# Performance work log

Measured on AMD Instinct MI355X. Metric: run time of the kernel, lower is better.

Reference implementation:

```python
import jax, jax.numpy as jnp
import numpy as np

B, S, V, E, HE, HD, MEL_D, MEL_T = 4096, 13, 276, 128, 256, 256, 80, 250

def setup_inputs() -> dict:
    key = jax.random.key(0)
    ks = jax.random.split(key, 20)
    p = lambda k, sh: (jax.random.normal(k, sh, dtype=jnp.float32) * 0.05)
    return {
        'text': jax.random.randint(ks[0], (B, S), 0, V),
        'surprisal': jax.random.normal(ks[1], (B, S), dtype=jnp.float32),
        'emb': p(ks[2], (V, E)),
        'sw': p(ks[3], (E, 1)), 'sb': p(ks[4], (E,)),
        'ew_ih': p(ks[5], (4 * HE, E)), 'ew_hh': p(ks[6], (4 * HE, HE)),
        'eb_ih': p(ks[7], (4 * HE,)), 'eb_hh': p(ks[8], (4 * HE,)),
        'aw': p(ks[9], (1, HD + HE)), 'ab': p(ks[10], (1,)),
        'dw_ih': p(ks[11], (4 * HD, E + HE)), 'dw_hh': p(ks[12], (4 * HD, HD)),
        'db_ih': p(ks[13], (4 * HD,)), 'db_hh': p(ks[14], (4 * HD,)),
        'f1w': p(ks[15], (1024, S * HD)), 'f1b': p(ks[16], (1024,)),
        'f2w': p(ks[17], (MEL_D * MEL_T, 1024)), 'f2b': p(ks[18], (MEL_D * MEL_T,)),
        'init_in': jnp.zeros((E,), dtype=jnp.float32),
    }

def _lstm_cell(x, h, c, w_ih, w_hh, b_ih, b_hh, H):
    # PyTorch gate order: i, f, g, o
    g = x @ w_ih.T + b_ih + h @ w_hh.T + b_hh
    i, f, gg, o = jnp.split(g, 4, axis=-1)
    c2 = jax.nn.sigmoid(f) * c + jax.nn.sigmoid(i) * jnp.tanh(gg)
    h2 = jax.nn.sigmoid(o) * jnp.tanh(c2)
    return h2, c2

def reference(text, surprisal, emb, sw, sb, ew_ih, ew_hh, eb_ih, eb_hh,
              aw, ab, dw_ih, dw_hh, db_ih, db_hh, f1w, f1b, f2w, f2b, init_in):
    # embedding + surprisal projection
    x = emb[text] + (surprisal[..., None] @ sw.T + sb)  # [B,S,E]

    # encoder LSTM over time
    def enc_step(carry, xt):
        h, c = carry
        h2, c2 = _lstm_cell(xt, h, c, ew_ih, ew_hh, eb_ih, eb_hh, HE)
        return (h2, c2), h2
    h0 = jnp.zeros((B, HE), dtype=x.dtype)
    (h_n, c_n), enc_seq = jax.lax.scan(enc_step, (h0, h0), jnp.swapaxes(x, 0, 1))
    enc_out = jnp.swapaxes(enc_seq, 0, 1)  # [B,S,HE]

    # precompute encoder part of attention scores (constant across steps)
    aw_h, aw_e = aw[0, :HD], aw[0, HD:]
    enc_score = enc_out @ aw_e + ab[0]  # [B,S]

    dec_in = jnp.broadcast_to(init_in, (B, E))

    def dec_step(carry, _):
        h, c = carry
        scores = h @ aw_h + 0.0  # [B]
        w = jax.nn.softmax(scores[:, None] + enc_score, axis=1)  # [B,S]
        context = jnp.einsum('bs,bsh->bh', w, enc_out)
        xcat = jnp.concatenate([dec_in, context], axis=-1)
        h2, c2 = _lstm_cell(xcat, h, c, dw_ih, dw_hh, db_ih, db_hh, HD)
        return (h2, c2), h2
    _, dec_seq = jax.lax.scan(dec_step, (h_n, c_n), None, length=S)
    dec_out = jnp.swapaxes(dec_seq, 0, 1).reshape(B, S * HD)  # [B,13*256]

    hfc = jax.nn.relu(dec_out @ f1w.T + f1b)
    out = (hfc @ f2w.T + f2b).reshape(B, MEL_D, MEL_T)
    return out
```

## Files before the change

kernel.cpp:

```cpp
#include <hip/hip_runtime.h>
#include <hip/hip_bf16.h>
#include <stdint.h>
#include <stddef.h>

#define B 4096
#define S 13
#define NG 1024
#define MEL 20000
#define MELP 20224

typedef __attribute__((ext_vector_type(8))) short bf16x8;
typedef __attribute__((ext_vector_type(4))) float f32x4;

__device__ __forceinline__ void g2l16(void* lds, const void* g) {
    __builtin_amdgcn_global_load_lds(
        (const __attribute__((address_space(1))) void*)g,
        (__attribute__((address_space(3))) void*)lds, 16, 0, 0);
}

__device__ __forceinline__ float sigm(float x) { return 1.0f / (1.0f + expf(-x)); }
__device__ __forceinline__ float b2f(unsigned short u) {
    union { float f; unsigned int i; } x; x.i = ((unsigned)u) << 16; return x.f;
}
__device__ __forceinline__ unsigned short f2bu(float f) {
    __hip_bfloat16 h = __float2bfloat16(f);
    return *reinterpret_cast<unsigned short*>(&h);
}
__device__ __forceinline__ bf16x8 cvt8(f32x4 a, f32x4 b) {
    union { bf16x8 v; __hip_bfloat16 e[8]; } u;
    #pragma unroll
    for (int j = 0; j < 4; ++j) { u.e[j] = __float2bfloat16(a[j]); u.e[4 + j] = __float2bfloat16(b[j]); }
    return u.v;
}

__device__ __forceinline__ void swz_decode(int wg, int nwg, int nx, int& bx, int& by) {
    const int cpx = nwg >> 3;
    wg = (wg & 7) * cpx + (wg >> 3);
    const int gsz = nx * 4;
    const int grp = wg / gsz, rem = wg % gsz;
    by = grp * 4 + (rem & 3);
    bx = rem >> 2;
}

#define BAR() do { asm volatile("" ::: "memory"); \
    __builtin_amdgcn_s_barrier(); \
    __builtin_amdgcn_sched_barrier(0); } while (0)

#define P_DECL() \
    __shared__ __hip_bfloat16 As3[4][128 * 32]; \
    __shared__ __hip_bfloat16 Bs3[4][64 * 32]; \
    const int tid  = threadIdx.x; \
    const int lane = tid & 63; \
    const int wv   = tid >> 6; \
    const int l16  = lane & 15; \
    const int sr   = tid >> 2; \
    const int sc   = (((tid & 3) ^ ((tid >> 3) & 3)) << 3); \
    const int sl   = (((lane >> 4) ^ ((l16 >> 1) & 3)) << 3)

#define STG3(buf, k0) do { \
    g2l16(&As3[buf][sr * 32 + (tid & 3) * 8],         Ag + (size_t)sr * K + (k0) + sc); \
    g2l16(&As3[buf][(sr + 64) * 32 + (tid & 3) * 8],  Ag + (size_t)(sr + 64) * K + (k0) + sc); \
    g2l16(&Bs3[buf][sr * 32 + (tid & 3) * 8],         Wg + (size_t)sr * K + (k0) + sc); } while (0)

#define TILE3(cur, stg, k2, DO_STG) do { \
    const __hip_bfloat16* Ab = As3[cur]; \
    const __hip_bfloat16* Bb = Bs3[cur]; \
    bf16x8 af[2], bfr[4]; \
    _Pragma("unroll") for (int m = 0; m < 2; ++m) \
        af[m] = *(const bf16x8*)(Ab + (wv * 32 + m * 16 + l16) * 32 + sl); \
    _Pragma("unroll") for (int n = 0; n < 4; ++n) \
        bfr[n] = *(const bf16x8*)(Bb + (n * 16 + l16) * 32 + sl); \
    if (DO_STG) STG3(stg, k2); \
    __builtin_amdgcn_s_setprio(1); \
    _Pragma("unroll") for (int m = 0; m < 2; ++m) \
        _Pragma("unroll") for (int n = 0; n < 4; ++n) \
            acc[m][n] = __builtin_amdgcn_mfma_f32_16x16x32_bf16(af[m], bfr[n], acc[m][n], 0, 0, 0); \
    __builtin_amdgcn_s_setprio(0); \
} while (0)

#define PIPELINE(K) do { \
    const int nk = (K) >> 5; \
    STG3(0, 0); \
    STG3(1, 32); \
    STG3(2, 64); \
    asm volatile("s_waitcnt vmcnt(6)" ::: "memory"); \
    BAR(); \
    int cur = 0; \
    for (int t = 0; t < nk - 3; ++t) { \
        const int stg = (cur + 3) & 3; \
        TILE3(cur, stg, (t + 3) << 5, true); \
        asm volatile("s_waitcnt vmcnt(6)" ::: "memory"); \
        BAR(); \
        cur = (cur + 1) & 3; \
    } \
    TILE3(cur, 0, 0, false); \
    asm volatile("s_waitcnt vmcnt(3)" ::: "memory"); \
    BAR(); \
    cur = (cur + 1) & 3; \
    TILE3(cur, 0, 0, false); \
    asm volatile("s_waitcnt vmcnt(0)" ::: "memory"); \
    BAR(); \
    cur = (cur + 1) & 3; \
    TILE3(cur, 0, 0, false); \
} while (0)

__global__ __launch_bounds__(256, 2) void gemm3(
    const __hip_bfloat16* __restrict__ A,
    const __hip_bfloat16* __restrict__ W,
    const float* __restrict__ bias,
    float* __restrict__ Cf,
    __hip_bfloat16* __restrict__ Cbf,
    int N, int K, int ldc, int relu, int nx)
{
    P_DECL();
    int bx, by;
    swz_decode(blockIdx.x, gridDim.x, nx, bx, by);
    const int brow = by * 128, bcol = bx * 64;
    const __hip_bfloat16* Ag = A + (size_t)brow * K;
    const __hip_bfloat16* Wg = W + (size_t)bcol * K;
    f32x4 acc[2][4] = {};

    PIPELINE(K);

    const int r4 = (lane >> 4) * 4;
    #pragma unroll
    for (int m = 0; m < 2; ++m) {
        #pragma unroll
        for (int n = 0; n < 4; ++n) {
            const int col = bcol + n * 16 + l16;
            if (col >= N) continue;
            const float bv = bias ? bias[col] : 0.0f;
            #pragma unroll
            for (int r = 0; r < 4; ++r) {
                const int row = brow + wv * 32 + m * 16 + r4 + r;
                float v = acc[m][n][r] + bv;
                if (relu) v = v > 0.0f ? v : 0.0f;
                if (Cf)  Cf[(size_t)row * ldc + col] = v;
                if (Cbf) Cbf[(size_t)row * ldc + col] = __float2bfloat16(v);
            }
        }
    }
}

__global__ __launch_bounds__(256, 2) void gemm_lstm3(
    const __hip_bfloat16* __restrict__ A,
    const __hip_bfloat16* __restrict__ W,
    const float* __restrict__ bias,
    float* __restrict__ c,
    float* __restrict__ hf,
    __hip_bfloat16* __restrict__ hb1, int s1,
    __hip_bfloat16* __restrict__ hb2, int s2,
    int K,
    const float* __restrict__ aw,
    float* __restrict__ score)
{
    P_DECL();
    int bx, by;
    swz_decode(blockIdx.x, gridDim.x, 16, bx, by);
    const int brow = by * 128, bcol = bx * 64;
    const __hip_bfloat16* Ag = A + (size_t)brow * K;
    const __hip_bfloat16* Wg = W + (size_t)bcol * K;
    f32x4 acc[2][4] = {};

    PIPELINE(K);

    const int r4 = (lane >> 4) * 4;
    const int unit = bx * 16 + l16;
    const float b0 = bias[bcol + l16];
    const float b1 = bias[bcol + 16 + l16];
    const float b2 = bias[bcol + 32 + l16];
    const float b3 = bias[bcol + 48 + l16];
    const float awe = score ? aw[256 + unit] : 0.0f;
    float ps[2][4];
    #pragma unroll
    for (int m = 0; m < 2; ++m) {
        #pragma unroll
        for (int r = 0; r < 4; ++r) {
            const int row = brow + wv * 32 + m * 16 + r4 + r;
            const float gi = acc[m][0][r] + b0;
            const float gf = acc[m][1][r] + b1;
            const float gg = acc[m][2][r] + b2;
            const float go = acc[m][3][r] + b3;
            const size_t ci = (size_t)row * 256 + unit;
            const float c2 = sigm(gf) * c[ci] + sigm(gi) * tanhf(gg);
            const float h2 = sigm(go) * tanhf(c2);
            c[ci] = c2;
            if (hf) hf[ci] = h2;
            ps[m][r] = h2 * awe;
            const __hip_bfloat16 hb = __float2bfloat16(h2);
            hb1[(size_t)row * s1 + unit] = hb;
            if (hb2) hb2[(size_t)row * s2 + unit] = hb;
        }
    }
    if (score) {
        #pragma unroll
        for (int m = 0; m < 2; ++m) {
            #pragma unroll
            for (int r = 0; r < 4; ++r) {
                float v = ps[m][r];
                v += __shfl_xor(v, 1);
                v += __shfl_xor(v, 2);
                v += __shfl_xor(v, 4);
                v += __shfl_xor(v, 8);
                if (l16 == 0) {
                    const int row = brow + wv * 32 + m * 16 + r4 + r;
                    atomicAdd(&score[(size_t)row * S], v);
                }
            }
        }
    }
}

__global__ __launch_bounds__(512, 2) void gemm256(
    const __hip_bfloat16* __restrict__ A,
    const __hip_bfloat16* __restrict__ W,
    const float* __restrict__ bias,
    float* __restrict__ Cf,
    int N, int K, int ldc, int nx)
{
    __shared__ __hip_bfloat16 As[4][256 * 32];
    __shared__ __hip_bfloat16 Bs[4][256 * 32];
    const int tid  = threadIdx.x;
    const int lane = tid & 63;
    const int wv = tid >> 6, wr = wv >> 2, wc = wv & 3;
    const int l16 = lane & 15;
    int bx, by;
    {
        int wg = blockIdx.x; const int nwg = gridDim.x;
        const int cpx = nwg >> 3;
        wg = (wg & 7) * cpx + (wg >> 3);
        const int gsz = nx * 2;
        const int grp = wg / gsz, rem = wg % gsz;
        by = grp * 2 + (rem & 1);
        bx = rem >> 1;
    }
    const int brow = by * 256, bcol = bx * 256;
    const __hip_bfloat16* Ag = A + (size_t)brow * K;
    const __hip_bfloat16* Wg = W + (size_t)bcol * K;
    const int sr = tid >> 2;
    const int sc = (((tid & 3) ^ ((tid >> 3) & 3)) << 3);
    const int sd = tid * 8;
    const int sl = (((lane >> 4) ^ ((l16 >> 1) & 3)) << 3);
    f32x4 acc[8][4] = {};
    const int nk = K >> 5;

    #define STG_A(buf, k0) do { \
        g2l16(&As[buf][sd],        Ag + (size_t)sr * K + (k0) + sc);         \
        g2l16(&As[buf][4096 + sd], Ag + (size_t)(sr + 128) * K + (k0) + sc); } while (0)
    #define STG_B(buf, k0) do { \
        g2l16(&Bs[buf][sd],        Wg + (size_t)sr * K + (k0) + sc);         \
        g2l16(&Bs[buf][4096 + sd], Wg + (size_t)(sr + 128) * K + (k0) + sc); } while (0)

    #define TILE(cur, stg, k2, DO_STG) do {                                    \
        const __hip_bfloat16* Ab = As[cur];                                    \
        const __hip_bfloat16* Bb = Bs[cur];                                    \
        bf16x8 bfr[4], af[4];                                                  \
        _Pragma("unroll") for (int n = 0; n < 4; ++n)                          \
            bfr[n] = *(const bf16x8*)(Bb + (wc * 64 + n * 16 + l16) * 32 + sl);\
        _Pragma("unroll") for (int m = 0; m < 4; ++m)                          \
            af[m] = *(const bf16x8*)(Ab + (wr * 128 + m * 16 + l16) * 32 + sl);\
        if (DO_STG) STG_A(stg, k2);                                            \
        BAR();                                                                 \
        __builtin_amdgcn_s_setprio(1);                                         \
        _Pragma("unroll") for (int m = 0; m < 4; ++m)                          \
            _Pragma("unroll") for (int n = 0; n < 4; ++n)                      \
                acc[m][n] = __builtin_amdgcn_mfma_f32_16x16x32_bf16(           \
                    af[m], bfr[n], acc[m][n], 0, 0, 0);                        \
        __builtin_amdgcn_s_setprio(0);                                         \
        BAR();                                                                 \
        _Pragma("unroll") for (int m = 0; m < 4; ++m)                          \
            af[m] = *(const bf16x8*)(Ab + (wr * 128 + (m + 4) * 16 + l16) * 32 + sl); \
        if (DO_STG) STG_B(stg, k2);                                            \
        BAR();                                                                 \
        __builtin_amdgcn_s_setprio(1);                                         \
        _Pragma("unroll") for (int m = 0; m < 4; ++m)                          \
            _Pragma("unroll") for (int n = 0; n < 4; ++n)                      \
                acc[m + 4][n] = __builtin_amdgcn_mfma_f32_16x16x32_bf16(       \
                    af[m], bfr[n], acc[m + 4][n], 0, 0, 0);                    \
        __builtin_amdgcn_s_setprio(0);                                         \
    } while (0)

    STG_A(0, 0);  STG_B(0, 0);
    STG_A(1, 32); STG_B(1, 32);
    STG_A(2, 64); STG_B(2, 64);
    asm volatile("s_waitcnt vmcnt(8)" ::: "memory");
    BAR();
    int cur = 0;
    for (int t = 0; t < nk - 3; ++t) {
        const int stg = (cur + 3) & 3;
        TILE(cur, stg, (t + 3) << 5, true);
        asm volatile("s_waitcnt vmcnt(8)" ::: "memory");
        BAR();
        cur = (cur + 1) & 3;
    }
    TILE(cur, 0, 0, false);
    asm volatile("s_waitcnt vmcnt(4)" ::: "memory");
    BAR();
    cur = (cur + 1) & 3;
    TILE(cur, 0, 0, false);
    asm volatile("s_waitcnt vmcnt(0)" ::: "memory");
    BAR();
    cur = (cur + 1) & 3;
    TILE(cur, 0, 0, false);

    const int r4 = (lane >> 4) * 4;
    #pragma unroll
    for (int m = 0; m < 8; ++m) {
        #pragma unroll
        for (int n = 0; n < 4; ++n) {
            const int col = bcol + wc * 64 + n * 16 + l16;
            if (col >= N) continue;
            const float bv = bias[col];
            #pragma unroll
            for (int r = 0; r < 4; ++r) {
                const int row = brow + wr * 128 + m * 16 + r4 + r;
                Cf[(size_t)row * ldc + col] = acc[m][n][r] + bv;
            }
        }
    }
}

__device__ __forceinline__ int unperm(int np) {
    const int u = ((np >> 6) << 4) + (np & 15);
    const int g = (np >> 4) & 3;
    return g * 256 + u;
}

#define N_W2   ((long long)MELP * 1024 / 8)
#define N_W1   ((long long)NG * 3328 / 8)
#define N_WE   ((long long)NG * 384 / 8)
#define N_WD   ((long long)NG * 512 / 8)
#define N_EMB  ((long long)B * S * 32)
#define N_INIT ((long long)B * 256)
#define N_F2B  ((long long)MELP)
#define N_BP   ((long long)NG)
#define N_ES   ((long long)B * S)
#define N_PREP (N_W2 + N_W1 + N_WE + N_WD + N_EMB + N_INIT + N_F2B + N_BP + N_ES)

__global__ void prep_all(
    const int* __restrict__ text, const float* __restrict__ surp,
    const float* __restrict__ emb, const float* __restrict__ sw,
    const float* __restrict__ sb,
    const float* __restrict__ ew_ih, const float* __restrict__ ew_hh,
    const float* __restrict__ eb_ih, const float* __restrict__ eb_hh,
    const float* __restrict__ dw_ih, const float* __restrict__ dw_hh,
    const float* __restrict__ db_ih, const float* __restrict__ db_hh,
    const float* __restrict__ f1w, const float* __restrict__ f2w,
    const float* __restrict__ f2b, const float* __restrict__ init_in,
    const float* __restrict__ ab,
    __hip_bfloat16* __restrict__ Wenc, __hip_bfloat16* __restrict__ Wdec,
    __hip_bfloat16* __restrict__ W1, __hip_bfloat16* __restrict__ W2,
    float* __restrict__ f2bp, float* __restrict__ be, float* __restrict__ bd,
    __hip_bfloat16* __restrict__ xall, float* __restrict__ c_buf,
    float* __restrict__ enc_score)
{
    long long id = (long long)blockIdx.x * 256 + threadIdx.x;
    if (id < N_W2) {
        const long long i8 = id * 8;
        bf16x8 v;
        if (i8 < (long long)MEL * 1024) {
            v = cvt8(*(const f32x4*)(f2w + i8), *(const f32x4*)(f2w + i8 + 4));
        } else {
            union { bf16x8 w; __hip_bfloat16 e[8]; } u;
            #pragma unroll
            for (int j = 0; j < 8; ++j) u.e[j] = __float2bfloat16(0.0f);
            v = u.w;
        }
        *(bf16x8*)(W2 + i8) = v;
        return;
    }
    id -= N_W2;
    if (id < N_W1) {
        const long long i8 = id * 8;
        *(bf16x8*)(W1 + i8) = cvt8(*(const f32x4*)(f1w + i8), *(const f32x4*)(f1w + i8 + 4));
        return;
    }
    id -= N_W1;
    if (id < N_WE) {
        const int idx = (int)(id * 8);
        const int np = idx / 384, k = idx % 384;
        const int n = unperm(np);
        const float* src = (k < 128) ? (ew_ih + n * 128 + k) : (ew_hh + n * 256 + (k - 128));
        *(bf16x8*)(Wenc + idx) = cvt8(*(const f32x4*)src, *(const f32x4*)(src + 4));
        return;
    }
    id -= N_WE;
    if (id < N_WD) {
        const int idx = (int)(id * 8);
        const int np = idx / 512, k = idx % 512;
        const int n = unperm(np);
        const float* src = (k < 256) ? (dw_ih + n * 384 + 128 + k) : (dw_hh + n * 256 + (k - 256));
        *(bf16x8*)(Wdec + idx) = cvt8(*(const f32x4*)src, *(const f32x4*)(src + 4));
        return;
    }
    id -= N_WD;
    if (id < N_EMB) {
        const int idx = (int)id;
        const int jj = (idx & 31) * 4;
        const int rest = idx >> 5;
        const int b = rest % B;
        const int s = rest / B;
        const float sp = surp[b * S + s];
        const f32x4 e4 = *(const f32x4*)(emb + (size_t)text[b * S + s] * 128 + jj);
        const f32x4 w4 = *(const f32x4*)(sw + jj);
        const f32x4 b4 = *(const f32x4*)(sb + jj);
        __hip_bfloat16* dst = xall + ((size_t)s * B + b) * 384 + jj;
        #pragma unroll
        for (int i = 0; i < 4; ++i) dst[i] = __float2bfloat16(e4[i] + sp * w4[i] + b4[i]);
        return;
    }
    id -= N_EMB;
    if (id < N_INIT) {
        const int idx = (int)id;
        c_buf[idx] = 0.0f;
        const int b = idx >> 8, jj = idx & 255;
        xall[(size_t)b * 384 + 128 + jj] = __float2bfloat16(0.0f);
        return;
    }
    id -= N_INIT;
    if (id < N_F2B) {
        const int idx = (int)id;
        f2bp[idx] = (idx < MEL) ? f2b[idx] : 0.0f;
        return;
    }
    id -= N_F2B;
    if (id < N_BP) {
        const int np = (int)id;
        const int n = unperm(np);
        be[np] = eb_ih[n] + eb_hh[n];
        float s = db_ih[n] + db_hh[n];
        for (int k = 0; k < 128; ++k) s += dw_ih[n * 384 + k] * init_in[k];
        bd[np] = s;
        return;
    }
    id -= N_BP;
    if (id < N_ES) {
        enc_score[id] = ab[0];
        return;
    }
}

__global__ void attn_kernel(const float* __restrict__ h, const __hip_bfloat16* __restrict__ enc_out,
                            const float* __restrict__ enc_score, const float* __restrict__ aw,
                            __hip_bfloat16* __restrict__ decA) {
    int b = (blockIdx.x * 256 + threadIdx.x) >> 6;
    int lane = threadIdx.x & 63;
    if (b >= B) return;
    const f32x4 h4 = *(const f32x4*)(h + (size_t)b * 256 + lane * 4);
    const f32x4 a4 = *(const f32x4*)(aw + lane * 4);
    float s = h4[0] * a4[0] + h4[1] * a4[1] + h4[2] * a4[2] + h4[3] * a4[3];
    #pragma unroll
    for (int off = 1; off < 64; off <<= 1) s += __shfl_xor(s, off);
    float sc[S], mx = -1e30f;
    #pragma unroll
    for (int t = 0; t < S; ++t) { sc[t] = s + enc_score[b * S + t]; mx = fmaxf(mx, sc[t]); }
    float sum = 0.0f;
    #pragma unroll
    for (int t = 0; t < S; ++t) { sc[t] = expf(sc[t] - mx); sum += sc[t]; }
    float inv = 1.0f / sum;
    float ctx[4] = {0.f, 0.f, 0.f, 0.f};
    #pragma unroll
    for (int t = 0; t < S; ++t) {
        const ushort4 e4 = *(const ushort4*)(enc_out + ((size_t)b * S + t) * 256 + lane * 4);
        float w = sc[t] * inv;
        ctx[0] += w * b2f(e4.x); ctx[1] += w * b2f(e4.y);
        ctx[2] += w * b2f(e4.z); ctx[3] += w * b2f(e4.w);
    }
    ushort4 o4;
    o4.x = f2bu(ctx[0]);
    o4.y = f2bu(ctx[1]);
    o4.z = f2bu(ctx[2]);
    o4.w = f2bu(ctx[3]);
    *(ushort4*)(decA + (size_t)b * 512 + lane * 4) = o4;
}

#define CDIV(a, b) (((a) + (b) - 1) / (b))

extern "C" void kernel_launch(void* const* d_in, const int* in_sizes, int n_in,
                              void* d_out, int out_size, void* d_ws, size_t ws_size,
                              hipStream_t stream) {
    const int*   text    = (const int*)  d_in[0];
    const float* surp    = (const float*)d_in[1];
    const float* emb     = (const float*)d_in[2];
    const float* sw      = (const float*)d_in[3];
    const float* sb      = (const float*)d_in[4];
    const float* ew_ih   = (const float*)d_in[5];
    const float* ew_hh   = (const float*)d_in[6];
    const float* eb_ih   = (const float*)d_in[7];
    const float* eb_hh   = (const float*)d_in[8];
    const float* aw      = (const float*)d_in[9];
    const float* ab      = (const float*)d_in[10];
    const float* dw_ih   = (const float*)d_in[11];
    const float* dw_hh   = (const float*)d_in[12];
    const float* db_ih   = (const float*)d_in[13];
    const float* db_hh   = (const float*)d_in[14];
    const float* f1w     = (const float*)d_in[15];
    const float* f1b     = (const float*)d_in[16];
    const float* f2w     = (const float*)d_in[17];
    const float* f2b     = (const float*)d_in[18];
    const float* init_in = (const float*)d_in[19];
    float* out = (float*)d_out;

    char* p = (char*)d_ws;
    auto alloc = [&](size_t bytes) {
        void* r = (void*)p;
        p += (bytes + 255) & ~(size_t)255;
        return r;
    };
    __hip_bfloat16* Wenc      = (__hip_bfloat16*)alloc((size_t)NG * 384 * 2);
    __hip_bfloat16* Wdec      = (__hip_bfloat16*)alloc((size_t)NG * 512 * 2);
    __hip_bfloat16* W1        = (__hip_bfloat16*)alloc((size_t)NG * 3328 * 2);
    __hip_bfloat16* W2        = (__hip_bfloat16*)alloc((size_t)MELP * 1024 * 2);
    float*          f2bp      = (float*)alloc((size_t)MELP * 4);
    float*          be        = (float*)alloc((size_t)NG * 4);
    float*          bd        = (float*)alloc((size_t)NG * 4);
    __hip_bfloat16* xall      = (__hip_bfloat16*)alloc((size_t)S * B * 384 * 2);
    __hip_bfloat16* enc_out   = (__hip_bfloat16*)alloc((size_t)B * S * 256 * 2);
    float*          enc_score = (float*)alloc((size_t)B * S * 4);
    float*          c_buf     = (float*)alloc((size_t)B * 256 * 4);
    float*          h_buf     = (float*)alloc((size_t)B * 256 * 4);
    __hip_bfloat16* decA      = (__hip_bfloat16*)alloc((size_t)B * 512 * 2);
    __hip_bfloat16* dec_out   = (__hip_bfloat16*)alloc((size_t)B * 3328 * 2);
    __hip_bfloat16* hfc       = (__hip_bfloat16*)alloc((size_t)B * 1024 * 2);
    (void)ws_size; (void)in_sizes; (void)n_in; (void)out_size;

    prep_all<<<(int)CDIV(N_PREP, 256), 256, 0, stream>>>(
        text, surp, emb, sw, sb, ew_ih, ew_hh, eb_ih, eb_hh,
        dw_ih, dw_hh, db_ih, db_hh, f1w, f2w, f2b, init_in, ab,
        Wenc, Wdec, W1, W2, f2bp, be, bd, xall, c_buf, enc_score);

    for (int t = 0; t < S; ++t) {
        __hip_bfloat16* hb1; int s1;
        if (t < S - 1) { hb1 = xall + ((size_t)(t + 1) * B * 384) + 128; s1 = 384; }
        else           { hb1 = decA + 256; s1 = 512; }
        float* hf = (t == S - 1) ? h_buf : (float*)nullptr;
        gemm_lstm3<<<512, 256, 0, stream>>>(
            xall + (size_t)t * B * 384, Wenc, be, c_buf, hf,
            hb1, s1, enc_out + (size_t)t * 256, S * 256, 384,
            aw, enc_score + t);
    }

    for (int t = 0; t < S; ++t) {
        attn_kernel<<<CDIV(B * 64, 256), 256, 0, stream>>>(h_buf, enc_out, enc_score, aw, decA);
        gemm_lstm3<<<512, 256, 0, stream>>>(
            decA, Wdec, bd, c_buf, h_buf,
            decA + 256, 512, dec_out + (size_t)t * 256, 3328, 512,
            aw, (float*)nullptr);
    }

    gemm3<<<(NG / 64) * (B / 128), 256, 0, stream>>>(
        dec_out, W1, f1b, (float*)nullptr, hfc, NG, 3328, NG, 1, NG / 64);

    gemm256<<<(MELP / 256) * (B / 256), 512, 0, stream>>>(
        hfc, W2, f2bp, out, MEL, 1024, MEL, MELP / 256);
}
```

Before: 732.4 us.

## Hoist step-invariant decoder attention context and its input projection out of loop

The decoder attention term h@aw_h adds the same value to every sequence position, so softmax cancels it. The context vector is therefore the same at every decoder step. The code now computes the context once, then runs one GEMM that projects it through the context half of the decoder input weights with the bias folded in. Each decoder step becomes a K=256 recurrent GEMM that adds the precomputed fp32 gate contribution, and the per-step attention kernel and fp32 h buffer writes go away. The cost is a 16MB fp32 gctx tensor that every step must reread, plus split weight buffers and double-buffered bf16 hidden states.

New measurement: 618.7 us. 15.5% less time.

```diff
diff --git a/kernel.cpp b/kernel.cpp
--- a/kernel.cpp
+++ b/kernel.cpp
@@ -147,7 +147,6 @@
     const __hip_bfloat16* __restrict__ W,
     const float* __restrict__ bias,
     float* __restrict__ c,
-    float* __restrict__ hf,
     __hip_bfloat16* __restrict__ hb1, int s1,
     __hip_bfloat16* __restrict__ hb2, int s2,
     int K,
@@ -185,11 +184,10 @@
             const float c2 = sigm(gf) * c[ci] + sigm(gi) * tanhf(gg);
             const float h2 = sigm(go) * tanhf(c2);
             c[ci] = c2;
-            if (hf) hf[ci] = h2;
             ps[m][r] = h2 * awe;
             const __hip_bfloat16 hb = __float2bfloat16(h2);
             hb1[(size_t)row * s1 + unit] = hb;
-            if (hb2) hb2[(size_t)row * s2 + unit] = hb;
+            hb2[(size_t)row * s2 + unit] = hb;
         }
     }
     if (score) {
@@ -207,6 +205,48 @@
                     atomicAdd(&score[(size_t)row * S], v);
                 }
             }
+        }
+    }
+}
+
+__global__ __launch_bounds__(256, 2) void gemm_lstm_dec(
+    const __hip_bfloat16* __restrict__ A,
+    const __hip_bfloat16* __restrict__ W,
+    const float* __restrict__ gctx,
+    float* __restrict__ c,
+    __hip_bfloat16* __restrict__ hb1,
+    __hip_bfloat16* __restrict__ hb2, int s2,
+    int K)
+{
+    P_DECL();
+    int bx, by;
+    swz_decode(blockIdx.x, gridDim.x, 16, bx, by);
+    const int brow = by * 128, bcol = bx * 64;
+    const __hip_bfloat16* Ag = A + (size_t)brow * K;
+    const __hip_bfloat16* Wg = W + (size_t)bcol * K;
+    f32x4 acc[2][4] = {};
+
+    PIPELINE(K);
+
+    const int r4 = (lane >> 4) * 4;
+    const int unit = bx * 16 + l16;
+    #pragma unroll
+    for (int m = 0; m < 2; ++m) {
+        #pragma unroll
+        for (int r = 0; r < 4; ++r) {
+            const int row = brow + wv * 32 + m * 16 + r4 + r;
+            const float* g = gctx + (size_t)row * NG + bcol;
+            const float gi = acc[m][0][r] + g[l16];
+            const float gf = acc[m][1][r] + g[16 + l16];
+            const float gg = acc[m][2][r] + g[32 + l16];
+            const float go = acc[m][3][r] + g[48 + l16];
+            const size_t ci = (size_t)row * 256 + unit;
+            const float c2 = sigm(gf) * c[ci] + sigm(gi) * tanhf(gg);
+            const float h2 = sigm(go) * tanhf(c2);
+            c[ci] = c2;
+            const __hip_bfloat16 hb = __float2bfloat16(h2);
+            hb1[(size_t)row * 256 + unit] = hb;
+            hb2[(size_t)row * s2 + unit] = hb;
         }
     }
 }
@@ -348,7 +388,8 @@
     const float* __restrict__ f1w, const float* __restrict__ f2w,
     const float* __restrict__ f2b, const float* __restrict__ init_in,
     const float* __restrict__ ab,
-    __hip_bfloat16* __restrict__ Wenc, __hip_bfloat16* __restrict__ Wdec,
+    __hip_bfloat16* __restrict__ Wenc,
+    __hip_bfloat16* __restrict__ Wdc, __hip_bfloat16* __restrict__ Wdh,
     __hip_bfloat16* __restrict__ W1, __hip_bfloat16* __restrict__ W2,
     float* __restrict__ f2bp, float* __restrict__ be, float* __restrict__ bd,
     __hip_bfloat16* __restrict__ xall, float* __restrict__ c_buf,
@@ -389,8 +430,13 @@
         const int idx = (int)(id * 8);
         const int np = idx / 512, k = idx % 512;
         const int n = unperm(np);
-        const float* src = (k < 256) ? (dw_ih + n * 384 + 128 + k) : (dw_hh + n * 256 + (k - 256));
-        *(bf16x8*)(Wdec + idx) = cvt8(*(const f32x4*)src, *(const f32x4*)(src + 4));
+        if (k < 256) {
+            const float* src = dw_ih + n * 384 + 128 + k;
+            *(bf16x8*)(Wdc + np * 256 + k) = cvt8(*(const f32x4*)src, *(const f32x4*)(src + 4));
+        } else {
+            const float* src = dw_hh + n * 256 + (k - 256);
+            *(bf16x8*)(Wdh + np * 256 + (k - 256)) = cvt8(*(const f32x4*)src, *(const f32x4*)(src + 4));
+        }
         return;
     }
     id -= N_WD;
@@ -440,38 +486,29 @@
     }
 }
 
-__global__ void attn_kernel(const float* __restrict__ h, const __hip_bfloat16* __restrict__ enc_out,
-                            const float* __restrict__ enc_score, const float* __restrict__ aw,
-                            __hip_bfloat16* __restrict__ decA) {
+__global__ void attn_once(const __hip_bfloat16* __restrict__ enc_out,
+                          const float* __restrict__ enc_score,
+                          __hip_bfloat16* __restrict__ ctx) {
     int b = (blockIdx.x * 256 + threadIdx.x) >> 6;
     int lane = threadIdx.x & 63;
     if (b >= B) return;
-    const f32x4 h4 = *(const f32x4*)(h + (size_t)b * 256 + lane * 4);
-    const f32x4 a4 = *(const f32x4*)(aw + lane * 4);
-    float s = h4[0] * a4[0] + h4[1] * a4[1] + h4[2] * a4[2] + h4[3] * a4[3];
-    #pragma unroll
-    for (int off = 1; off < 64; off <<= 1) s += __shfl_xor(s, off);
     float sc[S], mx = -1e30f;
     #pragma unroll
-    for (int t = 0; t < S; ++t) { sc[t] = s + enc_score[b * S + t]; mx = fmaxf(mx, sc[t]); }
+    for (int t = 0; t < S; ++t) { sc[t] = enc_score[b * S + t]; mx = fmaxf(mx, sc[t]); }
     float sum = 0.0f;
     #pragma unroll
     for (int t = 0; t < S; ++t) { sc[t] = expf(sc[t] - mx); sum += sc[t]; }
-    float inv = 1.0f / sum;
-    float ctx[4] = {0.f, 0.f, 0.f, 0.f};
+    const float inv = 1.0f / sum;
+    float c0 = 0.f, c1 = 0.f, c2 = 0.f, c3 = 0.f;
     #pragma unroll
     for (int t = 0; t < S; ++t) {
         const ushort4 e4 = *(const ushort4*)(enc_out + ((size_t)b * S + t) * 256 + lane * 4);
-        float w = sc[t] * inv;
-        ctx[0] += w * b2f(e4.x); ctx[1] += w * b2f(e4.y);
-        ctx[2] += w * b2f(e4.z); ctx[3] += w * b2f(e4.w);
-    }
-    ushort4 o4;
-    o4.x = f2bu(ctx[0]);
-    o4.y = f2bu(ctx[1]);
-    o4.z = f2bu(ctx[2]);
-    o4.w = f2bu(ctx[3]);
-    *(ushort4*)(decA + (size_t)b * 512 + lane * 4) = o4;
+        const float w = sc[t] * inv;
+        c0 += w * b2f(e4.x); c1 += w * b2f(e4.y);
+        c2 += w * b2f(e4.z); c3 += w * b2f(e4.w);
+    }
+    ushort4 o4 = { f2bu(c0), f2bu(c1), f2bu(c2), f2bu(c3) };
+    *(ushort4*)(ctx + (size_t)b * 256 + lane * 4) = o4;
 }
 
 #define CDIV(a, b) (((a) + (b) - 1) / (b))
@@ -508,7 +545,8 @@
         return r;
     };
     __hip_bfloat16* Wenc      = (__hip_bfloat16*)alloc((size_t)NG * 384 * 2);
-    __hip_bfloat16* Wdec      = (__hip_bfloat16*)alloc((size_t)NG * 512 * 2);
+    __hip_bfloat16* Wdc       = (__hip_bfloat16*)alloc((size_t)NG * 256 * 2);
+    __hip_bfloat16* Wdh       = (__hip_bfloat16*)alloc((size_t)NG * 256 * 2);
     __hip_bfloat16* W1        = (__hip_bfloat16*)alloc((size_t)NG * 3328 * 2);
     __hip_bfloat16* W2        = (__hip_bfloat16*)alloc((size_t)MELP * 1024 * 2);
     float*          f2bp      = (float*)alloc((size_t)MELP * 4);
@@ -518,8 +556,9 @@
     __hip_bfloat16* enc_out   = (__hip_bfloat16*)alloc((size_t)B * S * 256 * 2);
     float*          enc_score = (float*)alloc((size_t)B * S * 4);
     float*          c_buf     = (float*)alloc((size_t)B * 256 * 4);
-    float*          h_buf     = (float*)alloc((size_t)B * 256 * 4);
-    __hip_bfloat16* decA      = (__hip_bfloat16*)alloc((size_t)B * 512 * 2);
+    __hip_bfloat16* ctx       = (__hip_bfloat16*)alloc((size_t)B * 256 * 2);
+    float*          gctx      = (float*)alloc((size_t)B * NG * 4);
+    __hip_bfloat16* hdec      = (__hip_bfloat16*)alloc((size_t)2 * B * 256 * 2);
     __hip_bfloat16* dec_out   = (__hip_bfloat16*)alloc((size_t)B * 3328 * 2);
     __hip_bfloat16* hfc       = (__hip_bfloat16*)alloc((size_t)B * 1024 * 2);
     (void)ws_size; (void)in_sizes; (void)n_in; (void)out_size;
@@ -527,25 +566,27 @@
     prep_all<<<(int)CDIV(N_PREP, 256), 256, 0, stream>>>(
         text, surp, emb, sw, sb, ew_ih, ew_hh, eb_ih, eb_hh,
         dw_ih, dw_hh, db_ih, db_hh, f1w, f2w, f2b, init_in, ab,
-        Wenc, Wdec, W1, W2, f2bp, be, bd, xall, c_buf, enc_score);
+        Wenc, Wdc, Wdh, W1, W2, f2bp, be, bd, xall, c_buf, enc_score);
 
     for (int t = 0; t < S; ++t) {
         __hip_bfloat16* hb1; int s1;
         if (t < S - 1) { hb1 = xall + ((size_t)(t + 1) * B * 384) + 128; s1 = 384; }
-        else           { hb1 = decA + 256; s1 = 512; }
-        float* hf = (t == S - 1) ? h_buf : (float*)nullptr;
+        else           { hb1 = hdec; s1 = 256; }
         gemm_lstm3<<<512, 256, 0, stream>>>(
-            xall + (size_t)t * B * 384, Wenc, be, c_buf, hf,
+            xall + (size_t)t * B * 384, Wenc, be, c_buf,
             hb1, s1, enc_out + (size_t)t * 256, S * 256, 384,
             aw, enc_score + t);
     }
 
+    attn_once<<<CDIV(B * 64, 256), 256, 0, stream>>>(enc_out, enc_score, ctx);
+    gemm3<<<(NG / 64) * (B / 128), 256, 0, stream>>>(
+        ctx, Wdc, bd, gctx, (__hip_bfloat16*)nullptr, NG, 256, NG, 0, NG / 64);
+
     for (int t = 0; t < S; ++t) {
-        attn_kernel<<<CDIV(B * 64, 256), 256, 0, stream>>>(h_buf, enc_out, enc_score, aw, decA);
-        gemm_lstm3<<<512, 256, 0, stream>>>(
-            decA, Wdec, bd, c_buf, h_buf,
-            decA + 256, 512, dec_out + (size_t)t * 256, 3328, 512,
-            aw, (float*)nullptr);
+        gemm_lstm_dec<<<512, 256, 0, stream>>>(
+            hdec + (size_t)(t & 1) * B * 256, Wdh, gctx, c_buf,
+            hdec + (size_t)((t + 1) & 1) * B * 256,
+            dec_out + (size_t)t * 256, 3328, 256);
     }
 
     gemm3<<<(NG / 64) * (B / 128), 256, 0, stream>>>(
```
